# Kernel optimization log

Hardware: AMD Instinct MI355X
Metric: run time of the kernel (lower is better)

The kernel has to match this reference:

```python
import jax, jax.numpy as jnp
import numpy as np

INF = 1e30  # sentinel for 'unreached' cost
MAX_ITERS = 512


def setup_inputs() -> dict:
    key = jax.random.key(0)
    img = jax.random.uniform(key, (3, 2048, 2048), dtype=jnp.float32)
    return {"img": img}


def _sobel_mag(gray):
    # gray: [H,W] -> gradient magnitude [H,W] (the 'processing_filter')
    kx = jnp.array([[-1.0, 0.0, 1.0], [-2.0, 0.0, 2.0], [-1.0, 0.0, 1.0]], gray.dtype)
    k = jnp.stack([kx, kx.T])[:, None]  # [2,1,3,3]
    g = jax.lax.conv_general_dilated(gray[None, None], k, (1, 1), 'SAME')[0]  # [2,H,W]
    return jnp.sqrt(g[0] ** 2 + g[1] ** 2)


def _neighbor_min(c):
    # min over 4-connected neighbors, INF padding at borders
    big_r = jnp.full((1, c.shape[1]), INF, c.dtype)
    big_c = jnp.full((c.shape[0], 1), INF, c.dtype)
    n = jnp.concatenate([big_r, c[:-1]], 0)
    s = jnp.concatenate([c[1:], big_r], 0)
    w = jnp.concatenate([big_c, c[:, :-1]], 1)
    e = jnp.concatenate([c[:, 1:], big_c], 1)
    return jnp.minimum(jnp.minimum(n, s), jnp.minimum(w, e))


def _relax(cost, img):
    # minimax-path (flood-level) relaxation: cost[p] = min(cost[p], max(min_nbr_cost, img[p]))
    return jnp.minimum(cost, jnp.maximum(_neighbor_min(cost), img))


def _watershed2(img, markers):
    # marker-based watershed on topography `img` with labels {1,2}.
    # Label of p = argmin over seed sets of the minimax path cost (flooding level),
    # which matches skimage.segmentation.watershed region assignment (4-connectivity).
    c1 = jnp.where(markers == 1, img, jnp.float32(INF))
    c2 = jnp.where(markers == 2, img, jnp.float32(INF))

    def cond(st):
        _, _, i, ch = st
        return jnp.logical_and(ch, i < MAX_ITERS)

    def body(st):
        c1, c2, i, _ = st
        n1 = _relax(c1, img)
        n2 = _relax(c2, img)
        ch = jnp.logical_or(jnp.any(n1 < c1), jnp.any(n2 < c2))
        return n1, n2, i + 1, ch

    c1, c2, _, _ = jax.lax.while_loop(cond, body, (c1, c2, jnp.int32(0), jnp.bool_(True)))
    return jnp.where(c2 < c1, jnp.float32(2.0), jnp.float32(1.0))


def _forward(img):
    gray = jnp.einsum('chw,c->hw', img, jnp.array([0.2989, 0.587, 0.114], img.dtype))
    filter_res = _sobel_mag(gray)  # [H,W]
    q_hi = jnp.quantile(filter_res, 0.9925)
    q_lo = jnp.quantile(filter_res, 0.9825)
    # torch sets 2 first, then 1, so pixels satisfying both end up as 1
    markers = jnp.where(filter_res <= q_lo, 1, jnp.where(filter_res >= q_hi, 2, 0))
    labels = _watershed2(gray, markers)[None]  # [1,H,W], values in {1,2}
    labels = labels - labels.min()
    return labels / labels.max()


def reference(img):
    return _forward(img)
```

## Files before the change

### kernel.cpp

```cpp
#include <hip/hip_runtime.h>
#include <hip/hip_cooperative_groups.h>

#define HH 2048
#define WW 2048
#define NPX (HH*WW)
#define INFV 1e30f
#define TS 128
#define NT 16
#define NTL 256
#define CY 32

namespace cg = cooperative_groups;

__device__ __forceinline__ void BARL(){
  __builtin_amdgcn_sched_barrier(0);
  asm volatile("s_waitcnt lgkmcnt(0)" ::: "memory");
  __builtin_amdgcn_s_barrier();
  __builtin_amdgcn_sched_barrier(0);
}

__device__ __forceinline__ float sobel_at(const float* __restrict__ g, int y, int x){
  float a00,a01,a02,a10,a12,a20,a21,a22;
  if (y>0 && y<HH-1 && x>0 && x<WW-1){
    const float* p = g + (size_t)(y-1)*WW + x;
    a00=p[-1]; a01=p[0]; a02=p[1];
    p += WW;   a10=p[-1];          a12=p[1];
    p += WW;   a20=p[-1]; a21=p[0]; a22=p[1];
  } else {
    auto at=[&](int yy,int xx)->float{
      return (yy<0||yy>=HH||xx<0||xx>=WW)?0.0f:g[(size_t)yy*WW+xx];
    };
    a00=at(y-1,x-1); a01=at(y-1,x); a02=at(y-1,x+1);
    a10=at(y,  x-1);                a12=at(y,  x+1);
    a20=at(y+1,x-1); a21=at(y+1,x); a22=at(y+1,x+1);
  }
  float gx = __fadd_rn(__fadd_rn(__fsub_rn(a02,a00), __fmul_rn(2.0f,__fsub_rn(a12,a10))), __fsub_rn(a22,a20));
  float gy = __fadd_rn(__fadd_rn(__fsub_rn(a20,a00), __fmul_rn(2.0f,__fsub_rn(a21,a01))), __fsub_rn(a22,a02));
  return sqrtf(__fadd_rn(__fmul_rn(gx,gx),__fmul_rn(gy,gy)));
}

__global__ void gray_kernel(const float* __restrict__ img, float* __restrict__ gray){
  const float* R=img; const float* G=img+NPX; const float* B=img+2*(size_t)NPX;
  for (int i=blockIdx.x*blockDim.x+threadIdx.x; i<NPX; i+=gridDim.x*blockDim.x){
    gray[i] = __fadd_rn(__fadd_rn(__fmul_rn(0.2989f,R[i]),__fmul_rn(0.587f,G[i])),__fmul_rn(0.114f,B[i]));
  }
}

__global__ void sobel_hist1(const float* __restrict__ gray, float* __restrict__ fr,
                            unsigned* __restrict__ hist){
  __shared__ unsigned h[4*2048];
  for (int i=threadIdx.x;i<4*2048;i+=blockDim.x) h[i]=0;
  __syncthreads();
  const int rep=(threadIdx.x&3)*2048;
  for (int i=blockIdx.x*blockDim.x+threadIdx.x; i<NPX; i+=gridDim.x*blockDim.x){
    int y=i>>11, x=i&(WW-1);
    float f=sobel_at(gray,y,x);
    fr[i]=f;
    unsigned key=__float_as_uint(f);
    atomicAdd(&h[rep+(key>>21)],1u);
  }
  __syncthreads();
  for (int i=threadIdx.x;i<2048;i+=blockDim.x){
    unsigned s=h[i]+h[i+2048]+h[i+4096]+h[i+6144];
    if (s) atomicAdd(&hist[i],s);
  }
}

__global__ void hist_l2(const float* __restrict__ fr, const unsigned* __restrict__ sel1,
                        unsigned* __restrict__ hist2){
  __shared__ unsigned h[4*2048];
  __shared__ unsigned sb[4];
  if (threadIdx.x<4) sb[threadIdx.x]=sel1[threadIdx.x];
  for (int i=threadIdx.x;i<4*2048;i+=blockDim.x) h[i]=0;
  __syncthreads();
  for (int i=blockIdx.x*blockDim.x+threadIdx.x; i<NPX; i+=gridDim.x*blockDim.x){
    unsigned key=__float_as_uint(fr[i]);
    unsigned b=key>>21, sub=(key>>10)&0x7FFu;
    #pragma unroll
    for (int k=0;k<4;++k) if (b==sb[k]) atomicAdd(&h[k*2048+sub],1u);
  }
  __syncthreads();
  for (int i=threadIdx.x;i<4*2048;i+=blockDim.x){ unsigned s=h[i]; if (s) atomicAdd(&hist2[i],s); }
}

__global__ void hist_l3(const float* __restrict__ fr, const unsigned* __restrict__ sel1,
                        const unsigned* __restrict__ sel2, unsigned* __restrict__ hist3){
  __shared__ unsigned h[4*1024];
  __shared__ unsigned pf[4];
  if (threadIdx.x<4) pf[threadIdx.x]=(sel1[threadIdx.x]<<11)|sel2[threadIdx.x];
  for (int i=threadIdx.x;i<4*1024;i+=blockDim.x) h[i]=0;
  __syncthreads();
  for (int i=blockIdx.x*blockDim.x+threadIdx.x; i<NPX; i+=gridDim.x*blockDim.x){
    unsigned key=__float_as_uint(fr[i]);
    unsigned p22=key>>10, sub=key&0x3FFu;
    #pragma unroll
    for (int k=0;k<4;++k) if (p22==pf[k]) atomicAdd(&h[k*1024+sub],1u);
  }
  __syncthreads();
  for (int i=threadIdx.x;i<4*1024;i+=blockDim.x){ unsigned s=h[i]; if (s) atomicAdd(&hist3[i],s); }
}

__global__ void scan_l1(const unsigned* __restrict__ hist, unsigned* __restrict__ sel1,
                        unsigned* __restrict__ rem1){
  __shared__ unsigned part[1024];
  const int t=threadIdx.x;
  unsigned a=hist[2*t], b=hist[2*t+1];
  part[t]=a+b; __syncthreads();
  for (int off=1;off<1024;off<<=1){
    unsigned add=(t>=off)?part[t-off]:0u; __syncthreads();
    part[t]+=add; __syncthreads();
  }
  unsigned before=(t>0)?part[t-1]:0u;
  const unsigned R[4]={4120902u,4120903u,4162845u,4162846u};
  unsigned cum=before;
  #pragma unroll
  for (int i=0;i<4;++i) if (R[i]>=cum && R[i]<cum+a){ sel1[i]=2*t;   rem1[i]=R[i]-cum; }
  cum+=a;
  #pragma unroll
  for (int i=0;i<4;++i) if (R[i]>=cum && R[i]<cum+b){ sel1[i]=2*t+1; rem1[i]=R[i]-cum; }
}

__global__ void scan_l2(const unsigned* __restrict__ hist2, const unsigned* __restrict__ rem1,
                        unsigned* __restrict__ sel2, unsigned* __restrict__ rem2){
  __shared__ unsigned part[1024];
  const int t=threadIdx.x;
  for (int i=0;i<4;++i){
    const unsigned* hh=hist2+i*2048;
    unsigned a=hh[2*t], b=hh[2*t+1];
    part[t]=a+b; __syncthreads();
    for (int off=1;off<1024;off<<=1){
      unsigned add=(t>=off)?part[t-off]:0u; __syncthreads();
      part[t]+=add; __syncthreads();
    }
    unsigned before=(t>0)?part[t-1]:0u;
    unsigned r=rem1[i], cum=before;
    if (r>=cum && r<cum+a){ sel2[i]=2*t;   rem2[i]=r-cum; }
    cum+=a;
    if (r>=cum && r<cum+b){ sel2[i]=2*t+1; rem2[i]=r-cum; }
    __syncthreads();
  }
}

__global__ void scan_l3(const unsigned* __restrict__ hist3, const unsigned* __restrict__ sel1,
                        const unsigned* __restrict__ sel2, const unsigned* __restrict__ rem2,
                        float* __restrict__ scal){
  __shared__ unsigned part[1024];
  __shared__ float vals[4];
  const int t=threadIdx.x;
  for (int i=0;i<4;++i){
    unsigned c=hist3[i*1024+t];
    part[t]=c; __syncthreads();
    for (int off=1;off<1024;off<<=1){
      unsigned add=(t>=off)?part[t-off]:0u; __syncthreads();
      part[t]+=add; __syncthreads();
    }
    unsigned before=(t>0)?part[t-1]:0u;
    unsigned r=rem2[i];
    if (r>=before && r<before+c){
      unsigned key=(sel1[i]<<21)|(sel2[i]<<10)|(unsigned)t;
      vals[i]=__uint_as_float(key);
    }
    __syncthreads();
  }
  if (t==0){
    scal[0]=__fadd_rn(__fmul_rn(vals[0],0.25f),__fmul_rn(vals[1],0.75f));
    scal[1]=__fadd_rn(__fmul_rn(vals[2],0.25f),__fmul_rn(vals[3],0.75f));
  }
}

__global__ void init_cost(const float* __restrict__ gray, const float* frbuf,
                          const float* __restrict__ scal,
                          float* c1out, float* __restrict__ c2out){
  const float qlo=scal[0], qhi=scal[1];
  for (int i=blockIdx.x*blockDim.x+threadIdx.x; i<NPX; i+=gridDim.x*blockDim.x){
    float f=frbuf[i];
    float g=gray[i];
    bool m1 = (f<=qlo);
    bool m2 = (!m1) && (f>=qhi);
    c1out[i] = m1 ? g : INFV;
    c2out[i] = (m1|m2) ? g : INFV;
  }
}


#define HSCAN_LR(va,vb,gA,gB,hl) do{ \
  float ql_=gA[j], qh_=va[j]; \
  qh_=fminf(vb[j],fmaxf(gB[j],qh_)); ql_=fmaxf(gB[j],ql_); \
  _Pragma("unroll") \
  for (int d_=1;d_<64;d_<<=1){ \
    float pl_=__shfl_up(ql_,(unsigned)d_), ph_=__shfl_up(qh_,(unsigned)d_); \
    if (c>=d_){ qh_=fminf(qh_,fmaxf(ql_,ph_)); ql_=fmaxf(ql_,pl_); } \
  } \
  float E_=fminf(qh_,fmaxf(ql_,(hl))); \
  float In_=__shfl_up(E_,1u); if(c==0) In_=(hl); \
  float na_=fminf(va[j],fmaxf(gA[j],In_)); if(na_<va[j]){va[j]=na_;ch=true;} \
  float nb_=fminf(vb[j],fmaxf(gB[j],na_)); if(nb_<vb[j]){vb[j]=nb_;ch=true;} \
}while(0)

#define HSCAN_RL(va,vb,gA,gB,hr) do{ \
  float ql_=gB[j], qh_=vb[j]; \
  qh_=fminf(va[j],fmaxf(gA[j],qh_)); ql_=fmaxf(gA[j],ql_); \
  _Pragma("unroll") \
  for (int d_=1;d_<64;d_<<=1){ \
    float pl_=__shfl_down(ql_,(unsigned)d_), ph_=__shfl_down(qh_,(unsigned)d_); \
    if (c+d_<64){ qh_=fminf(qh_,fmaxf(ql_,ph_)); ql_=fmaxf(ql_,pl_); } \
  } \
  float E_=fminf(qh_,fmaxf(ql_,(hr))); \
  float In_=__shfl_down(E_,1u); if(c==63) In_=(hr); \
  float nb_=fminf(vb[j],fmaxf(gB[j],In_)); if(nb_<vb[j]){vb[j]=nb_;ch=true;} \
  float na_=fminf(va[j],fmaxf(gA[j],nb_)); if(na_<va[j]){va[j]=na_;ch=true;} \
}while(0)

#define VCOMP_DN(va,gA,Larr,Harr,XX) { float ql_=gA[0], qh_=va[0]; \
  _Pragma("unroll") for (int jj_=1;jj_<8;++jj_){ qh_=fminf(va[jj_],fmaxf(gA[jj_],qh_)); ql_=fmaxf(gA[jj_],ql_);} \
  Larr[w][XX]=ql_; Harr[w][XX]=qh_; }

#define VCOMP_UP(va,gA,Larr,Harr,XX) { float ql_=gA[7], qh_=va[7]; \
  _Pragma("unroll") for (int jj_=6;jj_>=0;--jj_){ qh_=fminf(va[jj_],fmaxf(gA[jj_],qh_)); ql_=fmaxf(gA[jj_],ql_);} \
  Larr[w][XX]=ql_; Harr[w][XX]=qh_; }

#define VAPPLY_DN(va,gA,Larr,XX) { float In_=Larr[w][XX]; \
  _Pragma("unroll") for (int jj_=0;jj_<8;++jj_){ float nv_=fminf(va[jj_],fmaxf(In_,gA[jj_])); if(nv_<va[jj_]){va[jj_]=nv_;ch=true;} In_=nv_; } }

#define VAPPLY_UP(va,gA,Larr,XX) { float In_=Larr[w][XX]; \
  _Pragma("unroll") for (int jj_=7;jj_>=0;--jj_){ float nv_=fminf(va[jj_],fmaxf(In_,gA[jj_])); if(nv_<va[jj_]){va[jj_]=nv_;ch=true;} In_=nv_; } }

#define CHAIN_DN(Harr,Larr,HT) { float E=HALO[HT][x]; \
  _Pragma("unroll") for (int b_=0;b_<16;++b_){ float I=E; E=fminf(Harr[b_][x],fmaxf(Larr[b_][x],I)); Larr[b_][x]=I; } }

#define CHAIN_UP(Harr,Larr,HB) { float E=HALO[HB][x]; \
  _Pragma("unroll") for (int b_=15;b_>=0;--b_){ float I=E; E=fminf(Harr[b_][x],fmaxf(Larr[b_][x],I)); Larr[b_][x]=I; } }

#define HFIELD(va,vb,IHL,IHR) do{ \
  _Pragma("unroll") \
  for (int j=0;j<8;++j){ \
    const int r_=(w<<3)|j; \
    const float hl=HALO[IHL][r_], hr=HALO[IHR][r_]; \
    { float la_=__shfl_up(vb[j],1u); if(c==0) la_=hl; \
      bool p_=__any((fminf(va[j],fmaxf(la_,ga[j]))<va[j])||(fminf(vb[j],fmaxf(va[j],gb[j]))<vb[j])); \
      if (p_){ HSCAN_LR(va,vb,ga,gb,hl); } } \
    { float ra_=__shfl_down(va[j],1u); if(c==63) ra_=hr; \
      bool p_=__any((fminf(vb[j],fmaxf(ra_,gb[j]))<vb[j])||(fminf(va[j],fmaxf(vb[j],ga[j]))<va[j])); \
      if (p_){ HSCAN_RL(va,vb,ga,gb,hr); } } \
  } \
}while(0)

#define ASTORE(p,v) __hip_atomic_store((p),(v),__ATOMIC_RELAXED,__HIP_MEMORY_SCOPE_AGENT)
#define ALOAD(p)    __hip_atomic_load((p),__ATOMIC_RELAXED,__HIP_MEMORY_SCOPE_AGENT)

__global__ void __launch_bounds__(1024,4)
ws_solve(float* __restrict__ c1g, const float* __restrict__ grayg, float* outg,
         int* __restrict__ flagIt)
{
  __shared__ float DNL1[16][128], DNH1[16][128], DNL2[16][128], DNH2[16][128];
  __shared__ float UPL1[16][128], UPH1[16][128], UPL2[16][128], UPH2[16][128];
  __shared__ float HALO[8][128];
  __shared__ int F1[3], F2[3];
  __shared__ int wflag;
  cg::grid_group grid = cg::this_grid();
  const int tid=threadIdx.x, w=tid>>6, c=tid&63;
  const int xcd=blockIdx.x&7, idx=blockIdx.x>>3;
  const int tx=((xcd&3)<<2)|(idx&3), ty=((xcd>>2)<<3)|(idx>>2);
  const int tile=ty*NT+tx;
  const int by=ty*TS, bx=tx*TS, x0=c<<1;
  float* EB1=outg;
  float* EB2=outg+(NTL*4*128);

  const int hx=tid&127, harr=tid>>7;
  const float* hsrc=nullptr;
  {
    const float* EB=(harr&1)?EB2:EB1;
    switch(harr>>1){
      case 0: if (ty>0)    hsrc=EB+((tile-NT)*4+1)*128+hx; break;
      case 1: if (ty<NT-1) hsrc=EB+((tile+NT)*4+0)*128+hx; break;
      case 2: if (tx>0)    hsrc=EB+((tile-1)*4+3)*128+hx;  break;
      default:if (tx<NT-1) hsrc=EB+((tile+1)*4+2)*128+hx;  break;
    }
  }

  float v1a[8],v1b[8],v2a[8],v2b[8],ga[8],gb[8];
  {
    size_t base=(size_t)(by+(w<<3))*WW + bx + x0;
    #pragma unroll
    for (int j=0;j<8;++j){
      float2 t1=*(const float2*)(c1g+base);
      float2 t2=*(const float2*)(outg+base);
      float2 tg=*(const float2*)(grayg+base);
      v1a[j]=t1.x; v1b[j]=t1.y; v2a[j]=t2.x; v2b[j]=t2.y; ga[j]=tg.x; gb[j]=tg.y;
      base+=(size_t)WW;
    }
  }
  grid.sync();

  if (w==0){ const int eb=(tile*4+0)*128;
    ASTORE(EB1+eb+x0,v1a[0]); ASTORE(EB1+eb+x0+1,v1b[0]);
    ASTORE(EB2+eb+x0,v2a[0]); ASTORE(EB2+eb+x0+1,v2b[0]); }
  if (w==15){ const int eb=(tile*4+1)*128;
    ASTORE(EB1+eb+x0,v1a[7]); ASTORE(EB1+eb+x0+1,v1b[7]);
    ASTORE(EB2+eb+x0,v2a[7]); ASTORE(EB2+eb+x0+1,v2b[7]); }
  if (c==0){ const int eb=(tile*4+2)*128+(w<<3);
    #pragma unroll
    for (int j=0;j<8;++j){ ASTORE(EB1+eb+j,v1a[j]); ASTORE(EB2+eb+j,v2a[j]); } }
  if (c==63){ const int eb=(tile*4+3)*128+(w<<3);
    #pragma unroll
    for (int j=0;j<8;++j){ ASTORE(EB1+eb+j,v1b[j]); ASTORE(EB2+eb+j,v2b[j]); } }
  HALO[harr][hx]=INFV;
  if (tid==0){ F1[0]=1;F2[0]=1;F1[1]=0;F2[1]=0;F1[2]=0;F2[2]=0; wflag=0; }
  float hv=0.0f; bool hvok=false;
  __threadfence();
  grid.sync();

  for (int win=0; win<192; ++win){
    for (int cyc=0; cyc<CY; ++cyc){
      const int gc=win*CY+cyc;
      const int cur=gc%3, nxt=(gc+1)%3, old=(gc+2)%3;
      if (hsrc){
        if (hvok && hv<HALO[harr][hx]){
          HALO[harr][hx]=hv;
          if (harr&1) F2[nxt]=1; else F1[nxt]=1;
        }
        hv=ALOAD(hsrc); hvok=true;
      }
      const int r1=F1[cur], r2=F2[cur];
      if (tid==0){ F1[old]=0; F2[old]=0; }
      if (!(r1|r2)){ BARL(); continue; }
      if (r1){
        VCOMP_DN(v1a,ga,DNL1,DNH1,x0) VCOMP_DN(v1b,gb,DNL1,DNH1,x0+1)
        VCOMP_UP(v1a,ga,UPL1,UPH1,x0) VCOMP_UP(v1b,gb,UPL1,UPH1,x0+1)
      }
      if (r2){
        VCOMP_DN(v2a,ga,DNL2,DNH2,x0) VCOMP_DN(v2b,gb,DNL2,DNH2,x0+1)
        VCOMP_UP(v2a,ga,UPL2,UPH2,x0) VCOMP_UP(v2b,gb,UPL2,UPH2,x0+1)
      }
      BARL();
      if (w<8){
        const int x=((w&1)<<6)|c;
        const bool go = (w>>2) ? (r2!=0) : (r1!=0);
        if (go){
          switch(w>>1){
            case 0: CHAIN_DN(DNH1,DNL1,0) break;
            case 1: CHAIN_UP(UPH1,UPL1,2) break;
            case 2: CHAIN_DN(DNH2,DNL2,1) break;
            default:CHAIN_UP(UPH2,UPL2,3) break;
          }
        }
      }
      BARL();
      bool chf1=false, chf2=false;
      if (r1){ bool ch=false;
        VAPPLY_DN(v1a,ga,DNL1,x0) VAPPLY_DN(v1b,gb,DNL1,x0+1)
        VAPPLY_UP(v1a,ga,UPL1,x0) VAPPLY_UP(v1b,gb,UPL1,x0+1)
        HFIELD(v1a,v1b,4,6);
        if (ch){ F1[nxt]=1; wflag=1; chf1=true; }
      }
      if (r2){ bool ch=false;
        VAPPLY_DN(v2a,ga,DNL2,x0) VAPPLY_DN(v2b,gb,DNL2,x0+1)
        VAPPLY_UP(v2a,ga,UPL2,x0) VAPPLY_UP(v2b,gb,UPL2,x0+1)
        HFIELD(v2a,v2b,5,7);
        if (ch){ F2[nxt]=1; wflag=1; chf2=true; }
      }
      if (chf1|chf2){
        if (w==0){ const int eb=(tile*4+0)*128;
          if(chf1){ ASTORE(EB1+eb+x0,v1a[0]); ASTORE(EB1+eb+x0+1,v1b[0]); }
          if(chf2){ ASTORE(EB2+eb+x0,v2a[0]); ASTORE(EB2+eb+x0+1,v2b[0]); } }
        if (w==15){ const int eb=(tile*4+1)*128;
          if(chf1){ ASTORE(EB1+eb+x0,v1a[7]); ASTORE(EB1+eb+x0+1,v1b[7]); }
          if(chf2){ ASTORE(EB2+eb+x0,v2a[7]); ASTORE(EB2+eb+x0+1,v2b[7]); } }
        if (c==0){ const int eb=(tile*4+2)*128+(w<<3);
          #pragma unroll
          for (int j=0;j<8;++j){ if(chf1)ASTORE(EB1+eb+j,v1a[j]); if(chf2)ASTORE(EB2+eb+j,v2a[j]); } }
        if (c==63){ const int eb=(tile*4+3)*128+(w<<3);
          #pragma unroll
          for (int j=0;j<8;++j){ if(chf1)ASTORE(EB1+eb+j,v1b[j]); if(chf2)ASTORE(EB2+eb+j,v2b[j]); } }
      }
      BARL();
    }
    if (tid==0 && wflag) atomicMax(flagIt,win+1);
    __threadfence();
    grid.sync();
    int fv=ALOAD(flagIt);
    if (fv<=win) break;
    if (tid==0) wflag=0;
    __syncthreads();
  }
  {
    size_t base=(size_t)(by+(w<<3))*WW + bx + x0;
    #pragma unroll
    for (int j=0;j<8;++j){
      float2 o; o.x=(v2a[j]<v1a[j])?1.0f:0.0f; o.y=(v2b[j]<v1b[j])?1.0f:0.0f;
      *(float2*)(outg+base)=o;
      base+=(size_t)WW;
    }
  }
}

extern "C" void kernel_launch(void* const* d_in, const int* in_sizes, int n_in,
                              void* d_out, int out_size, void* d_ws, size_t ws_size,
                              hipStream_t stream)
{
  const float* img=(const float*)d_in[0];
  float* out=(float*)d_out;
  char* wsb=(char*)d_ws;
  float* gray=(float*)wsb;
  float* c1  =(float*)(wsb + (size_t)NPX*4);
  unsigned* meta=(unsigned*)(wsb + (size_t)NPX*8);
  float* c2 = out;

  unsigned* hist1=meta;
  unsigned* hist2=meta+2048;
  unsigned* hist3=meta+10240;
  unsigned* sel1 =meta+14336;
  unsigned* rem1 =meta+14340;
  unsigned* sel2 =meta+14344;
  unsigned* rem2 =meta+14348;
  float*    scal =(float*)(meta+14352);
  int*      flagIt=(int*)(meta+14354);

  hipMemsetAsync(meta, 0, 14355*sizeof(unsigned), stream);
  hipLaunchKernelGGL(gray_kernel, dim3(4096), dim3(256), 0, stream, img, gray);
  hipLaunchKernelGGL(sobel_hist1, dim3(1024), dim3(256), 0, stream, gray, c1, hist1);
  hipLaunchKernelGGL(scan_l1, dim3(1), dim3(1024), 0, stream, hist1, sel1, rem1);
  hipLaunchKernelGGL(hist_l2, dim3(1024), dim3(256), 0, stream, c1, sel1, hist2);
  hipLaunchKernelGGL(scan_l2, dim3(1), dim3(1024), 0, stream, hist2, rem1, sel2, rem2);
  hipLaunchKernelGGL(hist_l3, dim3(1024), dim3(256), 0, stream, c1, sel1, sel2, hist3);
  hipLaunchKernelGGL(scan_l3, dim3(1), dim3(1024), 0, stream, hist3, sel1, sel2, rem2, scal);
  hipLaunchKernelGGL(init_cost, dim3(4096), dim3(256), 0, stream, gray, c1, scal, c1, c2);

  void* args[]={ (void*)&c1,(void*)&gray,(void*)&out,(void*)&flagIt };
  (void)hipLaunchCooperativeKernel(ws_solve, dim3(NTL), dim3(1024), args, 0, stream);
}
```

Before: 599.3 us.

## Split vertical/horizontal dirty flags and lengthen sync windows in watershed solver

Replaces the per-label dirty flag with separate vertical-pass and horizontal-pass flags, so each phase runs only when the other phase or a halo update could have changed its input. The cycle loop is unrolled by two, with double-buffered flags and two halo registers in place of the triple-buffered flag rotation. The window length grows from 32 to 128 cycles, which cuts the number of grid-wide syncs. In exchange, convergence may be detected later, adding up to a window of idle cycles, and the skip logic could miss propagation if the flag dependencies are wrong.

```diff
diff --git a/kernel.cpp b/kernel.cpp
--- a/kernel.cpp
+++ b/kernel.cpp
@@ -8,7 +8,7 @@
 #define TS 128
 #define NT 16
 #define NTL 256
-#define CY 32
+#define CY 128
 
 namespace cg = cooperative_groups;
 
@@ -248,6 +248,80 @@
 #define ASTORE(p,v) __hip_atomic_store((p),(v),__ATOMIC_RELAXED,__HIP_MEMORY_SCOPE_AGENT)
 #define ALOAD(p)    __hip_atomic_load((p),__ATOMIC_RELAXED,__HIP_MEMORY_SCOPE_AGENT)
 
+#define CYCLE(HV,CUR,NXT) do{ \
+  if (hsrc){ \
+    if (HV < HALO[harr][hx]){ \
+      HALO[harr][hx]=HV; \
+      if (harr<4){ if (harr&1) VN2[NXT]=1; else VN1[NXT]=1; } \
+      else       { if (harr&1) HN2[NXT]=1; else HN1[NXT]=1; } \
+    } \
+    HV=ALOAD(hsrc); \
+  } \
+  const int vn1=VN1[CUR], hn1=HN1[CUR], vn2=VN2[CUR], hn2=HN2[CUR]; \
+  if (!(vn1|hn1|vn2|hn2)){ \
+    BARL(); \
+  } else { \
+    if (vn1){ \
+      VCOMP_DN(v1a,ga,DNL1,DNH1,x0) VCOMP_DN(v1b,gb,DNL1,DNH1,x0+1) \
+      VCOMP_UP(v1a,ga,UPL1,UPH1,x0) VCOMP_UP(v1b,gb,UPL1,UPH1,x0+1) \
+    } \
+    if (vn2){ \
+      VCOMP_DN(v2a,ga,DNL2,DNH2,x0) VCOMP_DN(v2b,gb,DNL2,DNH2,x0+1) \
+      VCOMP_UP(v2a,ga,UPL2,UPH2,x0) VCOMP_UP(v2b,gb,UPL2,UPH2,x0+1) \
+    } \
+    BARL(); \
+    if (w<8){ \
+      const int x=((w&1)<<6)|c; \
+      const bool go = (w>>2) ? (vn2!=0) : (vn1!=0); \
+      if (go){ \
+        switch(w>>1){ \
+          case 0: CHAIN_DN(DNH1,DNL1,0) break; \
+          case 1: CHAIN_UP(UPH1,UPL1,2) break; \
+          case 2: CHAIN_DN(DNH2,DNL2,1) break; \
+          default:CHAIN_UP(UPH2,UPL2,3) break; \
+        } \
+      } \
+    } \
+    BARL(); \
+    bool chf1=false, chf2=false; \
+    if (vn1){ bool ch=false; \
+      VAPPLY_DN(v1a,ga,DNL1,x0) VAPPLY_DN(v1b,gb,DNL1,x0+1) \
+      VAPPLY_UP(v1a,ga,UPL1,x0) VAPPLY_UP(v1b,gb,UPL1,x0+1) \
+      if (ch){ chf1=true; HN1[NXT]=1; } \
+    } \
+    if (hn1){ bool ch=false; \
+      HFIELD(v1a,v1b,4,6); \
+      if (ch){ chf1=true; VN1[NXT]=1; } \
+    } \
+    if (vn2){ bool ch=false; \
+      VAPPLY_DN(v2a,ga,DNL2,x0) VAPPLY_DN(v2b,gb,DNL2,x0+1) \
+      VAPPLY_UP(v2a,ga,UPL2,x0) VAPPLY_UP(v2b,gb,UPL2,x0+1) \
+      if (ch){ chf2=true; HN2[NXT]=1; } \
+    } \
+    if (hn2){ bool ch=false; \
+      HFIELD(v2a,v2b,5,7); \
+      if (ch){ chf2=true; VN2[NXT]=1; } \
+    } \
+    if (chf1|chf2){ \
+      if (w==0){ const int eb=(tile*4+0)*128; \
+        if(chf1){ ASTORE(EB1+eb+x0,v1a[0]); ASTORE(EB1+eb+x0+1,v1b[0]); } \
+        if(chf2){ ASTORE(EB2+eb+x0,v2a[0]); ASTORE(EB2+eb+x0+1,v2b[0]); } } \
+      if (w==15){ const int eb=(tile*4+1)*128; \
+        if(chf1){ ASTORE(EB1+eb+x0,v1a[7]); ASTORE(EB1+eb+x0+1,v1b[7]); } \
+        if(chf2){ ASTORE(EB2+eb+x0,v2a[7]); ASTORE(EB2+eb+x0+1,v2b[7]); } } \
+      if (c==0){ const int eb=(tile*4+2)*128+(w<<3); \
+        _Pragma("unroll") \
+        for (int j=0;j<8;++j){ if(chf1)ASTORE(EB1+eb+j,v1a[j]); if(chf2)ASTORE(EB2+eb+j,v2a[j]); } } \
+      if (c==63){ const int eb=(tile*4+3)*128+(w<<3); \
+        _Pragma("unroll") \
+        for (int j=0;j<8;++j){ if(chf1)ASTORE(EB1+eb+j,v1b[j]); if(chf2)ASTORE(EB2+eb+j,v2b[j]); } } \
+      wflag=1; \
+    } \
+    if (tid==0){ VN1[CUR]=0; HN1[CUR]=0; VN2[CUR]=0; HN2[CUR]=0; } \
+    BARL(); \
+  } \
+}while(0)
+
 __global__ void __launch_bounds__(1024,4)
 ws_solve(float* __restrict__ c1g, const float* __restrict__ grayg, float* outg,
          int* __restrict__ flagIt)
@@ -255,7 +329,7 @@
   __shared__ float DNL1[16][128], DNH1[16][128], DNL2[16][128], DNH2[16][128];
   __shared__ float UPL1[16][128], UPH1[16][128], UPL2[16][128], UPH2[16][128];
   __shared__ float HALO[8][128];
-  __shared__ int F1[3], F2[3];
+  __shared__ int VN1[2],HN1[2],VN2[2],HN2[2];
   __shared__ int wflag;
   cg::grid_group grid = cg::this_grid();
   const int tid=threadIdx.x, w=tid>>6, c=tid&63;
@@ -305,75 +379,18 @@
     #pragma unroll
     for (int j=0;j<8;++j){ ASTORE(EB1+eb+j,v1b[j]); ASTORE(EB2+eb+j,v2b[j]); } }
   HALO[harr][hx]=INFV;
-  if (tid==0){ F1[0]=1;F2[0]=1;F1[1]=0;F2[1]=0;F1[2]=0;F2[2]=0; wflag=0; }
-  float hv=0.0f; bool hvok=false;
+  if (tid==0){ VN1[0]=1;HN1[0]=1;VN2[0]=1;HN2[0]=1;
+               VN1[1]=0;HN1[1]=0;VN2[1]=0;HN2[1]=0; wflag=0; }
   __threadfence();
   grid.sync();
 
-  for (int win=0; win<192; ++win){
-    for (int cyc=0; cyc<CY; ++cyc){
-      const int gc=win*CY+cyc;
-      const int cur=gc%3, nxt=(gc+1)%3, old=(gc+2)%3;
-      if (hsrc){
-        if (hvok && hv<HALO[harr][hx]){
-          HALO[harr][hx]=hv;
-          if (harr&1) F2[nxt]=1; else F1[nxt]=1;
-        }
-        hv=ALOAD(hsrc); hvok=true;
-      }
-      const int r1=F1[cur], r2=F2[cur];
-      if (tid==0){ F1[old]=0; F2[old]=0; }
-      if (!(r1|r2)){ BARL(); continue; }
-      if (r1){
-        VCOMP_DN(v1a,ga,DNL1,DNH1,x0) VCOMP_DN(v1b,gb,DNL1,DNH1,x0+1)
-        VCOMP_UP(v1a,ga,UPL1,UPH1,x0) VCOMP_UP(v1b,gb,UPL1,UPH1,x0+1)
-      }
-      if (r2){
-        VCOMP_DN(v2a,ga,DNL2,DNH2,x0) VCOMP_DN(v2b,gb,DNL2,DNH2,x0+1)
-        VCOMP_UP(v2a,ga,UPL2,UPH2,x0) VCOMP_UP(v2b,gb,UPL2,UPH2,x0+1)
-      }
-      BARL();
-      if (w<8){
-        const int x=((w&1)<<6)|c;
-        const bool go = (w>>2) ? (r2!=0) : (r1!=0);
-        if (go){
-          switch(w>>1){
-            case 0: CHAIN_DN(DNH1,DNL1,0) break;
-            case 1: CHAIN_UP(UPH1,UPL1,2) break;
-            case 2: CHAIN_DN(DNH2,DNL2,1) break;
-            default:CHAIN_UP(UPH2,UPL2,3) break;
-          }
-        }
-      }
-      BARL();
-      bool chf1=false, chf2=false;
-      if (r1){ bool ch=false;
-        VAPPLY_DN(v1a,ga,DNL1,x0) VAPPLY_DN(v1b,gb,DNL1,x0+1)
-        VAPPLY_UP(v1a,ga,UPL1,x0) VAPPLY_UP(v1b,gb,UPL1,x0+1)
-        HFIELD(v1a,v1b,4,6);
-        if (ch){ F1[nxt]=1; wflag=1; chf1=true; }
-      }
-      if (r2){ bool ch=false;
-        VAPPLY_DN(v2a,ga,DNL2,x0) VAPPLY_DN(v2b,gb,DNL2,x0+1)
-        VAPPLY_UP(v2a,ga,UPL2,x0) VAPPLY_UP(v2b,gb,UPL2,x0+1)
-        HFIELD(v2a,v2b,5,7);
-        if (ch){ F2[nxt]=1; wflag=1; chf2=true; }
-      }
-      if (chf1|chf2){
-        if (w==0){ const int eb=(tile*4+0)*128;
-          if(chf1){ ASTORE(EB1+eb+x0,v1a[0]); ASTORE(EB1+eb+x0+1,v1b[0]); }
-          if(chf2){ ASTORE(EB2+eb+x0,v2a[0]); ASTORE(EB2+eb+x0+1,v2b[0]); } }
-        if (w==15){ const int eb=(tile*4+1)*128;
-          if(chf1){ ASTORE(EB1+eb+x0,v1a[7]); ASTORE(EB1+eb+x0+1,v1b[7]); }
-          if(chf2){ ASTORE(EB2+eb+x0,v2a[7]); ASTORE(EB2+eb+x0+1,v2b[7]); } }
-        if (c==0){ const int eb=(tile*4+2)*128+(w<<3);
-          #pragma unroll
-          for (int j=0;j<8;++j){ if(chf1)ASTORE(EB1+eb+j,v1a[j]); if(chf2)ASTORE(EB2+eb+j,v2a[j]); } }
-        if (c==63){ const int eb=(tile*4+3)*128+(w<<3);
-          #pragma unroll
-          for (int j=0;j<8;++j){ if(chf1)ASTORE(EB1+eb+j,v1b[j]); if(chf2)ASTORE(EB2+eb+j,v2b[j]); } }
-      }
-      BARL();
+  float hvA=INFV, hvB=INFV;
+  if (hsrc){ hvA=ALOAD(hsrc); hvB=ALOAD(hsrc); }
+
+  for (int win=0; win<48; ++win){
+    for (int cyc=0; cyc<CY; cyc+=2){
+      CYCLE(hvA,0,1);
+      CYCLE(hvB,1,0);
     }
     if (tid==0 && wflag) atomicMax(flagIt,win+1);
     __threadfence();
```

Measured after the change: 609.5 us. No clear change (+1.7%).
